# Kernel optimization log

Hardware: AMD Instinct MI355X
Metric: run time of the kernel (lower is better)

Reference implementation:

```python
import jax, jax.numpy as jnp
import numpy as np


def _proj(x, W, b):
    # 1x1 conv == per-pixel dense: [B,H,W,Cin] @ [Cin,Cout] + [Cout]
    return jnp.einsum('bhwc,cd->bhwd', x, W) + b


def setup_inputs() -> dict:
    key = jax.random.key(0)
    ks = jax.random.split(key, 5)
    B, Wd, Hd, C = 8, 64, 64, 128
    scale = 1.0 / np.sqrt(C)
    inp = {'x': jax.random.normal(ks[0], (B, Wd, Hd, C), dtype=jnp.float32)}
    for i, name in enumerate(['f', 'g', 'h', 'v']):
        inp['W' + name] = jax.random.normal(ks[i + 1], (C, C), dtype=jnp.float32) * scale
        inp['b' + name] = jnp.zeros((C,), dtype=jnp.float32)
    return inp


def reference(x, Wf, bf, Wg, bg, Wh, bh, Wv, bv):
    B, W, H, C = x.shape
    N = W * H
    fx = _proj(x, Wf, bf).reshape(B, N, C)
    gx = _proj(x, Wg, bg).reshape(B, N, C)
    hx = _proj(x, Wh, bh).reshape(B, N, C)
    # alpha[b,n,m] = softmax over m of fx @ gx^T
    alpha = jax.nn.softmax(jnp.einsum('bnc,bmc->bnm', fx, gx), axis=-1)
    # o = hx^T @ alpha -> [B, C, N], then reshape to [B, W, H, C] (faithful to original)
    o = jnp.einsum('bnc,bnm->bcm', hx, alpha).reshape(B, W, H, C)
    return _proj(o, Wv, bv)
```

## Files before the change

kernel.cpp:

```cpp
#include <hip/hip_runtime.h>
#include <math.h>

#define NB 8
#define NN 4096
#define NC 128

typedef __attribute__((ext_vector_type(8)))  short bf16x8;
typedef __attribute__((ext_vector_type(4)))  float f32x4;
typedef __attribute__((ext_vector_type(16))) float f32x16;

#define L2E   1.4426950408889634f
#define SBIAS 43.2808512266689f

static __device__ __forceinline__ float fexp2(float x) { return __builtin_amdgcn_exp2f(x); }
static __device__ __forceinline__ float flog2(float x) { return __builtin_amdgcn_logf(x); }

static __device__ __forceinline__ unsigned short f2bf(float f) {
    unsigned u = __builtin_bit_cast(unsigned, f);
    return (unsigned short)((u + 0x7FFFu + ((u >> 16) & 1u)) >> 16);
}


__global__ __launch_bounds__(256) void k_proj(
    const float* __restrict__ x,
    const float* __restrict__ Wf, const float* __restrict__ bf,
    const float* __restrict__ Wg, const float* __restrict__ bg,
    const float* __restrict__ Wh, const float* __restrict__ bh,
    unsigned short* __restrict__ fb, unsigned short* __restrict__ gb,
    unsigned short* __restrict__ htb)
{
    const float* W; const float* bias;
    if (blockIdx.z == 0)      { W = Wf; bias = bf; }
    else if (blockIdx.z == 1) { W = Wg; bias = bg; }
    else                      { W = Wh; bias = bh; }

    __shared__ __align__(16) float ast[32 * 32];
    __shared__ __align__(16) float bs [32 * 128];

    const int tid = threadIdx.x;
    const int tx = tid & 31, ty = tid >> 5;
    const int r0 = blockIdx.x * 32;

    float acc[4][4] = {};

    for (int cc = 0; cc < 128; cc += 32) {
        __syncthreads();
        {
            int r = tid >> 3, c4 = tid & 7;
            float4 v = *(const float4*)&x[(size_t)(r0 + r) * NC + cc + c4 * 4];
            ast[(c4 * 4 + 0) * 32 + r] = v.x;
            ast[(c4 * 4 + 1) * 32 + r] = v.y;
            ast[(c4 * 4 + 2) * 32 + r] = v.z;
            ast[(c4 * 4 + 3) * 32 + r] = v.w;
        }
        #pragma unroll
        for (int i = 0; i < 4; i++) {
            int idx = tid + i * 256;
            *(float4*)&bs[idx * 4] = *(const float4*)&W[(size_t)cc * 128 + idx * 4];
        }
        __syncthreads();
        #pragma unroll
        for (int c = 0; c < 32; c++) {
            float4 a  = *(const float4*)&ast[c * 32 + ty * 4];
            float4 b4 = *(const float4*)&bs [c * 128 + tx * 4];
            acc[0][0] += a.x * b4.x; acc[0][1] += a.x * b4.y; acc[0][2] += a.x * b4.z; acc[0][3] += a.x * b4.w;
            acc[1][0] += a.y * b4.x; acc[1][1] += a.y * b4.y; acc[1][2] += a.y * b4.z; acc[1][3] += a.y * b4.w;
            acc[2][0] += a.z * b4.x; acc[2][1] += a.z * b4.y; acc[2][2] += a.z * b4.z; acc[2][3] += a.z * b4.w;
            acc[3][0] += a.w * b4.x; acc[3][1] += a.w * b4.y; acc[3][2] += a.w * b4.z; acc[3][3] += a.w * b4.w;
        }
    }

    float4 bb = *(const float4*)&bias[tx * 4];
    float bbv[4] = { bb.x, bb.y, bb.z, bb.w };

    if (blockIdx.z < 2) {
        unsigned short* out = (blockIdx.z == 0) ? fb : gb;
        const int kc = tx >> 2, hi2 = (tx >> 1) & 1, j0 = (tx & 1) * 4;
        const size_t base = ((size_t)(r0 >> 5) * 8 + kc) * 512;
        #pragma unroll
        for (int i = 0; i < 4; i++) {
            ushort4 v;
            v.x = f2bf(acc[i][0] + bbv[0]);
            v.y = f2bf(acc[i][1] + bbv[1]);
            v.z = f2bf(acc[i][2] + bbv[2]);
            v.w = f2bf(acc[i][3] + bbv[3]);
            int lane = (ty * 4 + i) + 32 * hi2;
            *(ushort4*)&out[base + (size_t)lane * 8 + j0] = v;
        }
    } else {
        const int b   = r0 >> 12;
        const int ncc = (r0 & (NN - 1)) >> 5;
        const int s   = ty >> 2, hj = (ty >> 1) & 1, jj0 = (ty & 1) * 4;
        const int cb  = tx >> 3;
        #pragma unroll
        for (int j = 0; j < 4; j++) {
            int c = tx * 4 + j;
            int lane = (c & 31) + 32 * hj;
            ushort4 v;
            v.x = f2bf(acc[0][j] + bbv[j]);
            v.y = f2bf(acc[1][j] + bbv[j]);
            v.z = f2bf(acc[2][j] + bbv[j]);
            v.w = f2bf(acc[3][j] + bbv[j]);
            size_t off = ((((size_t)(b * 4 + cb) * 128 + ncc) * 2 + s) * 64 + lane) * 8 + jj0;
            *(ushort4*)&htb[off] = v;
        }
    }
}

__global__ __launch_bounds__(512, 2) void k_stats(
    const unsigned short* __restrict__ fb, const unsigned short* __restrict__ gb,
    float* __restrict__ Cout)
{
    const int b = blockIdx.y;
    const int tid = threadIdx.x;
    const int w = tid >> 6;
    const int l = tid & 63;
    const int t = w & 1, q = w >> 1;
    const int nbase = blockIdx.x * 64 + t * 32;

    const size_t fbase = ((size_t)(b * 128 + (nbase >> 5)) * 8) * 512 + (size_t)l * 8;
    bf16x8 bfr[8];
    #pragma unroll
    for (int kc = 0; kc < 8; kc++)
        bfr[kc] = *(const bf16x8*)&fb[fbase + kc * 512];

    float sum = 0.f;
    for (int mt = 0; mt < 32; mt++) {
        const size_t gbase = ((size_t)(b * 128 + q * 32 + mt) * 8) * 512 + (size_t)l * 8;
        f32x16 S0 = {}; f32x16 S1 = {};
        #pragma unroll
        for (int kc = 0; kc < 8; kc += 2) {
            S0 = __builtin_amdgcn_mfma_f32_32x32x16_bf16(*(const bf16x8*)&gb[gbase + kc * 512], bfr[kc], S0, 0, 0, 0);
            S1 = __builtin_amdgcn_mfma_f32_32x32x16_bf16(*(const bf16x8*)&gb[gbase + (kc + 1) * 512], bfr[kc + 1], S1, 0, 0, 0);
        }
        #pragma unroll
        for (int r = 0; r < 16; r++)
            sum += fexp2(__builtin_fmaf(S0[r] + S1[r], L2E, -SBIAS));
    }

    sum += __shfl_xor(sum, 32, 64);

    __shared__ float red[8][32];
    if (l < 32) red[w][l] = sum;
    __syncthreads();
    if (q == 0 && l < 32) {
        float tot = red[t][l] + red[t + 2][l] + red[t + 4][l] + red[t + 6][l];
        Cout[(size_t)b * NN + nbase + l] = -(SBIAS + flog2(tot));
    }
}

__global__ __launch_bounds__(512, 2) void k_out(
    const unsigned short* __restrict__ fb, const unsigned short* __restrict__ gb,
    const unsigned short* __restrict__ htb, const float* __restrict__ Cn,
    float* __restrict__ O0, float* __restrict__ O1, float* __restrict__ O2,
    float* __restrict__ Od, int nsplit)
{
    const int b = blockIdx.z;
    const int tid = threadIdx.x;
    const int w = tid >> 6, l = tid & 63;
    const int lr = l & 31, hi = l >> 5;
    const int m0 = blockIdx.x * 256 + w * 32;

    const int chunks = (NN / 32) / nsplit;
    const int c0g = blockIdx.y * chunks;
    float* O = Od;
    if ((int)blockIdx.y + 1 < nsplit)
        O = (blockIdx.y == 0) ? O0 : ((blockIdx.y == 1) ? O1 : O2);

    const size_t gbase = ((size_t)(b * 128 + blockIdx.x * 8 + w) * 8) * 512 + (size_t)l * 8;
    bf16x8 gfr[8];
    #pragma unroll
    for (int kc = 0; kc < 8; kc++)
        gfr[kc] = *(const bf16x8*)&gb[gbase + kc * 512];

    const float* Cb = Cn + (size_t)b * NN;

    f32x16 acc[4] = { {}, {}, {}, {} };

    for (int nc = 0; nc < chunks; nc++) {
        const int ncg = c0g + nc;
        const int n0 = ncg * 32;

        const size_t fbase = ((size_t)(b * 128 + ncg) * 8) * 512 + (size_t)l * 8;
        bf16x8 fcur[8];
        #pragma unroll
        for (int kc = 0; kc < 8; kc++)
            fcur[kc] = *(const bf16x8*)&fb[fbase + kc * 512];

        bf16x8 hA[8];
        #pragma unroll
        for (int cb = 0; cb < 4; cb++) {
            const size_t hbase = ((((size_t)(b * 4 + cb) * 128 + ncg) * 2) * 64) * 8 + (size_t)l * 8;
            hA[2 * cb]     = *(const bf16x8*)&htb[hbase];
            hA[2 * cb + 1] = *(const bf16x8*)&htb[hbase + 512];
        }
        float4 Cv[4];
        #pragma unroll
        for (int q = 0; q < 4; q++)
            Cv[q] = *(const float4*)&Cb[n0 + q * 8 + hi * 4];

        f32x16 S0 = {}; f32x16 S1 = {};
        #pragma unroll
        for (int kc = 0; kc < 8; kc += 2) {
            S0 = __builtin_amdgcn_mfma_f32_32x32x16_bf16(fcur[kc], gfr[kc], S0, 0, 0, 0);
            S1 = __builtin_amdgcn_mfma_f32_32x32x16_bf16(fcur[kc + 1], gfr[kc + 1], S1, 0, 0, 0);
        }

        unsigned pk[8];
        #pragma unroll
        for (int p = 0; p < 8; p++) {
            int r0i = 2 * p, r1i = 2 * p + 1;
            float a0 = fexp2(__builtin_fmaf(S0[r0i] + S1[r0i], L2E, Cv[r0i >> 2][r0i & 3]));
            float a1 = fexp2(__builtin_fmaf(S0[r1i] + S1[r1i], L2E, Cv[r1i >> 2][r1i & 3]));
            asm("v_cvt_pk_bf16_f32 %0, %1, %2" : "=v"(pk[p]) : "v"(a0), "v"(a1));
        }
        unsigned part[8];
        #pragma unroll
        for (int p = 0; p < 8; p++)
            part[p] = (unsigned)__shfl_xor((int)pk[p], 32, 64);

        uint4 b0, b1;
        b0.x = hi ? part[2] : pk[0];
        b0.y = hi ? part[3] : pk[1];
        b0.z = hi ? pk[2]   : part[0];
        b0.w = hi ? pk[3]   : part[1];
        b1.x = hi ? part[6] : pk[4];
        b1.y = hi ? part[7] : pk[5];
        b1.z = hi ? pk[6]   : part[4];
        b1.w = hi ? pk[7]   : part[5];
        bf16x8 B0 = __builtin_bit_cast(bf16x8, b0);
        bf16x8 B1 = __builtin_bit_cast(bf16x8, b1);

        #pragma unroll
        for (int cb = 0; cb < 4; cb++) {
            acc[cb] = __builtin_amdgcn_mfma_f32_32x32x16_bf16(hA[2 * cb],     B0, acc[cb], 0, 0, 0);
            acc[cb] = __builtin_amdgcn_mfma_f32_32x32x16_bf16(hA[2 * cb + 1], B1, acc[cb], 0, 0, 0);
        }
    }

    #pragma unroll
    for (int cb = 0; cb < 4; cb++) {
        #pragma unroll
        for (int r = 0; r < 16; r++) {
            int row = (r & 3) + 8 * (r >> 2) + 4 * hi;
            O[((size_t)b * NC + cb * 32 + row) * NN + m0 + lr] = acc[cb][r];
        }
    }
}

__global__ __launch_bounds__(256) void k_vproj(
    float* __restrict__ o, const float* __restrict__ E0,
    const float* __restrict__ E1, const float* __restrict__ E2,
    const float* __restrict__ Wv, const float* __restrict__ bv, int nextra)
{
    __shared__ __align__(16) float ast[32 * 32];
    __shared__ __align__(16) float bs [32 * 128];

    const int tid = threadIdx.x;
    const int tx = tid & 31, ty = tid >> 5;
    const int r0 = blockIdx.x * 32;

    float acc[4][4] = {};

    for (int cc = 0; cc < 128; cc += 32) {
        __syncthreads();
        {
            int r = tid >> 3, c4 = tid & 7;
            size_t idx = (size_t)(r0 + r) * NC + cc + c4 * 4;
            float4 v = *(const float4*)&o[idx];
            if (nextra > 0) {
                float4 u = *(const float4*)&E0[idx];
                v.x += u.x; v.y += u.y; v.z += u.z; v.w += u.w;
            }
            if (nextra > 1) {
                float4 u = *(const float4*)&E1[idx];
                v.x += u.x; v.y += u.y; v.z += u.z; v.w += u.w;
            }
            if (nextra > 2) {
                float4 u = *(const float4*)&E2[idx];
                v.x += u.x; v.y += u.y; v.z += u.z; v.w += u.w;
            }
            ast[(c4 * 4 + 0) * 32 + r] = v.x;
            ast[(c4 * 4 + 1) * 32 + r] = v.y;
            ast[(c4 * 4 + 2) * 32 + r] = v.z;
            ast[(c4 * 4 + 3) * 32 + r] = v.w;
        }
        #pragma unroll
        for (int i = 0; i < 4; i++) {
            int idx = tid + i * 256;
            *(float4*)&bs[idx * 4] = *(const float4*)&Wv[(size_t)cc * 128 + idx * 4];
        }
        __syncthreads();
        #pragma unroll
        for (int c = 0; c < 32; c++) {
            float4 a  = *(const float4*)&ast[c * 32 + ty * 4];
            float4 b4 = *(const float4*)&bs [c * 128 + tx * 4];
            acc[0][0] += a.x * b4.x; acc[0][1] += a.x * b4.y; acc[0][2] += a.x * b4.z; acc[0][3] += a.x * b4.w;
            acc[1][0] += a.y * b4.x; acc[1][1] += a.y * b4.y; acc[1][2] += a.y * b4.z; acc[1][3] += a.y * b4.w;
            acc[2][0] += a.z * b4.x; acc[2][1] += a.z * b4.y; acc[2][2] += a.z * b4.z; acc[2][3] += a.z * b4.w;
            acc[3][0] += a.w * b4.x; acc[3][1] += a.w * b4.y; acc[3][2] += a.w * b4.z; acc[3][3] += a.w * b4.w;
        }
    }
    float4 bb = *(const float4*)&bv[tx * 4];
    #pragma unroll
    for (int i = 0; i < 4; i++) {
        float4 r;
        r.x = acc[i][0] + bb.x; r.y = acc[i][1] + bb.y;
        r.z = acc[i][2] + bb.z; r.w = acc[i][3] + bb.w;
        *(float4*)&o[(size_t)(r0 + ty * 4 + i) * NC + tx * 4] = r;
    }
}

extern "C" void kernel_launch(void* const* d_in, const int* in_sizes, int n_in,
                              void* d_out, int out_size, void* d_ws, size_t ws_size,
                              hipStream_t stream)
{
    const float* x  = (const float*)d_in[0];
    const float* Wf = (const float*)d_in[1];
    const float* bf = (const float*)d_in[2];
    const float* Wg = (const float*)d_in[3];
    const float* bg = (const float*)d_in[4];
    const float* Wh = (const float*)d_in[5];
    const float* bh = (const float*)d_in[6];
    const float* Wv = (const float*)d_in[7];
    const float* bv = (const float*)d_in[8];
    float* out = (float*)d_out;

    unsigned short* fbp = (unsigned short*)d_ws;
    unsigned short* gbp = fbp + (size_t)NB * NN * NC;
    unsigned short* htp = gbp + (size_t)NB * NN * NC;
    float* Cn = (float*)(htp + (size_t)NB * NN * NC);
    float* Opart = Cn + (size_t)NB * NN;
    const size_t osz = (size_t)NB * NC * NN;
    size_t base = (size_t)((char*)Opart - (char*)d_ws);
    int nsplit = 1;
    if (ws_size >= base + 3 * osz * 4) nsplit = 4;
    else if (ws_size >= base + osz * 4) nsplit = 2;
    float* O0 = Opart;
    float* O1 = Opart + osz;
    float* O2 = Opart + 2 * osz;

    k_proj<<<dim3(1024, 1, 3), 256, 0, stream>>>(x, Wf, bf, Wg, bg, Wh, bh, fbp, gbp, htp);

    k_stats<<<dim3(NN / 64, NB), 512, 0, stream>>>(fbp, gbp, Cn);

    k_out<<<dim3(NN / 256, nsplit, NB), 512, 0, stream>>>(fbp, gbp, htp, Cn, O0, O1, O2, out, nsplit);

    k_vproj<<<dim3(1024), 256, 0, stream>>>(out, O0, O1, O2, Wv, bv, nsplit - 1);
}
```

Measured before the change: 242.2 us.

## Stage f and h chunks through double-buffered LDS with register prefetch

Previously every wave in the block loaded the same f and h^T chunk fragments straight from global memory, so each chunk was read eight times per block. The block now loads each chunk once cooperatively, one 16-byte vector per thread, into a double-buffered LDS area, and prefetches the next chunk into registers while the current one is computed. Waves then read their MFMA fragments from LDS. This cuts redundant global and L2 traffic, but adds a __syncthreads per chunk and 32KB of LDS, which could limit occupancy at two blocks per CU.

Result: faster. 226.7 us (-6.4%).

```diff
diff --git a/kernel.cpp b/kernel.cpp
--- a/kernel.cpp
+++ b/kernel.cpp
@@ -161,6 +161,9 @@
     const int lr = l & 31, hi = l >> 5;
     const int m0 = blockIdx.x * 256 + w * 32;
 
+    __shared__ __align__(16) char ldsF[2][8192];
+    __shared__ __align__(16) char ldsH[2][8192];
+
     const int chunks = (NN / 32) / nsplit;
     const int c0g = blockIdx.y * chunks;
     float* O = Od;
@@ -175,24 +178,38 @@
 
     const float* Cb = Cn + (size_t)b * NN;
 
+    const size_t fstage0 = (size_t)b * 128 * 4096 + (size_t)tid * 8;
+    const int p = tid >> 6, pcb = p >> 1, ps = p & 1;
+    const size_t hstage0 = ((size_t)(b * 4 + pcb) * 256 + ps) * 512 + (size_t)(tid & 63) * 8;
+
     f32x16 acc[4] = { {}, {}, {}, {} };
 
+    uint4 fv = *(const uint4*)&fb[fstage0 + (size_t)c0g * 4096];
+    uint4 hv = *(const uint4*)&htb[hstage0 + (size_t)c0g * 1024];
+
     for (int nc = 0; nc < chunks; nc++) {
+        const int cur = nc & 1;
         const int ncg = c0g + nc;
         const int n0 = ncg * 32;
-
-        const size_t fbase = ((size_t)(b * 128 + ncg) * 8) * 512 + (size_t)l * 8;
+        const int ncgN = c0g + ((nc + 1 < chunks) ? nc + 1 : nc);
+
+        *(uint4*)(ldsF[cur] + tid * 16) = fv;
+        *(uint4*)(ldsH[cur] + tid * 16) = hv;
+        __syncthreads();
+
+        fv = *(const uint4*)&fb[fstage0 + (size_t)ncgN * 4096];
+        hv = *(const uint4*)&htb[hstage0 + (size_t)ncgN * 1024];
+
         bf16x8 fcur[8];
         #pragma unroll
         for (int kc = 0; kc < 8; kc++)
-            fcur[kc] = *(const bf16x8*)&fb[fbase + kc * 512];
+            fcur[kc] = *(const bf16x8*)(ldsF[cur] + kc * 1024 + l * 16);
 
         bf16x8 hA[8];
         #pragma unroll
         for (int cb = 0; cb < 4; cb++) {
-            const size_t hbase = ((((size_t)(b * 4 + cb) * 128 + ncg) * 2) * 64) * 8 + (size_t)l * 8;
-            hA[2 * cb]     = *(const bf16x8*)&htb[hbase];
-            hA[2 * cb + 1] = *(const bf16x8*)&htb[hbase + 512];
+            hA[2 * cb]     = *(const bf16x8*)(ldsH[cur] + (cb * 2 + 0) * 1024 + l * 16);
+            hA[2 * cb + 1] = *(const bf16x8*)(ldsH[cur] + (cb * 2 + 1) * 1024 + l * 16);
         }
         float4 Cv[4];
         #pragma unroll
@@ -208,16 +225,16 @@
 
         unsigned pk[8];
         #pragma unroll
-        for (int p = 0; p < 8; p++) {
-            int r0i = 2 * p, r1i = 2 * p + 1;
+        for (int pp = 0; pp < 8; pp++) {
+            int r0i = 2 * pp, r1i = 2 * pp + 1;
             float a0 = fexp2(__builtin_fmaf(S0[r0i] + S1[r0i], L2E, Cv[r0i >> 2][r0i & 3]));
             float a1 = fexp2(__builtin_fmaf(S0[r1i] + S1[r1i], L2E, Cv[r1i >> 2][r1i & 3]));
-            asm("v_cvt_pk_bf16_f32 %0, %1, %2" : "=v"(pk[p]) : "v"(a0), "v"(a1));
+            asm("v_cvt_pk_bf16_f32 %0, %1, %2" : "=v"(pk[pp]) : "v"(a0), "v"(a1));
         }
         unsigned part[8];
         #pragma unroll
-        for (int p = 0; p < 8; p++)
-            part[p] = (unsigned)__shfl_xor((int)pk[p], 32, 64);
+        for (int pp = 0; pp < 8; pp++)
+            part[pp] = (unsigned)__shfl_xor((int)pk[pp], 32, 64);
 
         uint4 b0, b1;
         b0.x = hi ? part[2] : pk[0];
```
